# Optimization experiments

Hardware: AMD Instinct MI355X
Metric: run time of the kernel (lower is better)

The kernel has to match this reference:

```python
import jax, jax.numpy as jnp
import numpy as np

B, H, L, DK = 16, 16, 2048, 64   # batch, heads, query len, head dim
LK = 4096                        # original key length
C = 10                           # num_clusters
LKS = 2 * int(np.log(LK))        # shrunk key length = 16


def _lin(x, w, b):
    # torch nn.Linear: y = x @ W^T + b
    return jnp.matmul(x, w.T) + b


def setup_inputs() -> dict:
    key = jax.random.key(0)
    ks = jax.random.split(key, 20)
    s = 0.05
    inp = {
        "Q": jax.random.normal(ks[0], (B, H, L, DK), jnp.float32),
        "K": jax.random.normal(ks[1], (B, H, LK, DK), jnp.float32),
        "V": jax.random.normal(ks[2], (B, H, LK, DK), jnp.float32),
        # shrink_k / shrink_v: Linear(l_k, 2*log(l_k))
        "shrink_k_w": jax.random.normal(ks[3], (LKS, LK), jnp.float32) * s,
        "shrink_k_b": jax.random.normal(ks[4], (LKS,), jnp.float32) * s,
        "shrink_v_w": jax.random.normal(ks[5], (LKS, LK), jnp.float32) * s,
        "shrink_v_b": jax.random.normal(ks[6], (LKS,), jnp.float32) * s,
        # proj_to_cluster_k: Linear(batch_size, num_clusters) + ReLU
        "proj_w": jax.random.normal(ks[7], (C, B), jnp.float32) * s,
        "proj_b": jax.random.normal(ks[8], (C,), jnp.float32) * s,
        "ck_w": jax.random.normal(ks[9], (C, C), jnp.float32) * s,
        "ck_b": jax.random.normal(ks[10], (C,), jnp.float32) * s,
        "cq_w": jax.random.normal(ks[11], (C, C), jnp.float32) * s,
        "cq_b": jax.random.normal(ks[12], (C,), jnp.float32) * s,
        "mu_w": jax.random.normal(ks[13], (C, C), jnp.float32) * s,
        "mu_b": jax.random.normal(ks[14], (C,), jnp.float32) * s,
        "sig_w": jax.random.normal(ks[15], (C, C), jnp.float32) * s,
        "sig_b": jax.random.normal(ks[16], (C,), jnp.float32) * s,
    }
    return inp


def reference(Q, K, V, shrink_k_w, shrink_k_b, shrink_v_w, shrink_v_b,
              proj_w, proj_b, ck_w, ck_b, cq_w, cq_b, mu_w, mu_b, sig_w, sig_b):
    b = Q.shape[0]
    # shrink along key sequence dim: (b,h,lk,d) -> (b,h,LKS,d)
    Ks = jnp.einsum('bhkd,sk->bhsd', K, shrink_k_w) + shrink_k_b[:, None]
    Vs = jnp.einsum('bhkd,sk->bhsd', V, shrink_v_w) + shrink_v_b[:, None]

    # pad + unfold over the batch dim: window j of K_padded[w:w+b]
    K_padded = jnp.concatenate([jnp.zeros_like(Ks), Ks[1:]], axis=0)  # (2b-1,h,LKS,d)
    idx = jnp.arange(b)[:, None] + jnp.arange(b)[None, :]             # (b, b)
    K_unfold = jnp.moveaxis(K_padded[idx], 1, -1)                     # (b,h,LKS,d,b)

    cluster_k_p = jax.nn.relu(_lin(K_unfold, proj_w, proj_b))         # (b,h,LKS,d,C)
    cluster_k = jax.nn.softmax(_lin(cluster_k_p, ck_w, ck_b), axis=-1)
    cluster_q = jax.nn.softmax(_lin(cluster_k_p, cq_w, cq_b), axis=-1)

    mu = _lin(cluster_q, mu_w, mu_b)
    sigma = jax.nn.softplus(_lin(cluster_q, sig_w, sig_b))
    # Normal log_prob
    log_prob = (-0.5 * jnp.square((cluster_k - mu) / sigma)
                - jnp.log(sigma) - 0.5 * jnp.log(2.0 * jnp.pi).astype(cluster_k.dtype))
    # torch CrossEntropyLoss with probability targets: class dim = dim 1 (= h)
    logp = jax.nn.log_softmax(cluster_q, axis=1)
    ce = -jnp.mean(jnp.sum(cluster_q * logp, axis=1))
    loss = -jnp.mean(log_prob) + ce

    # per-cluster masked mean over the last dim, vectorized over clusters.
    # where(argmax==i, cluster_q, 0).mean(-1) == onehot(argmax)[...,i] * mean(cluster_q,-1)
    masks = jax.nn.one_hot(jnp.argmax(cluster_q, axis=-1), C, dtype=cluster_q.dtype)  # (b,h,LKS,d,C)
    q_mean = jnp.mean(cluster_q, axis=-1)                                              # (b,h,LKS,d)
    q_sub = masks * q_mean[..., None]                                                  # (b,h,LKS,d,C)

    scores = jnp.einsum('bhqd,bhkdc->cbhqk', Q, q_sub)  # (C,b,h,l,LKS)
    final_score = jnp.max(scores, axis=0)               # (b,h,l,LKS)
    attn = jax.nn.softmax(final_score, axis=-1)
    context = jnp.einsum('bhqk,bhkd->bhqd', attn, Vs)   # (b,h,l,d)
    return context, loss
```

## Files before the change

kernel.cpp:

```cpp
#include <hip/hip_runtime.h>

#define KS_OFF 0
#define VS_OFF 262144
#define QM_OFF 524288
#define AM_OFF 786432
#define LP_OFF 1048576
#define CE_OFF 1048832

typedef __attribute__((ext_vector_type(8))) short short8;
typedef __attribute__((ext_vector_type(4))) float f32x4;

__device__ inline unsigned short bfb(float x) {
  unsigned u = __float_as_uint(x);
  return (unsigned short)((u + 0x7fffu + ((u >> 16) & 1u)) >> 16);
}
__device__ inline unsigned pk2(float a, float b) {
  return (unsigned)bfb(a) | ((unsigned)bfb(b) << 16);
}
__device__ inline float bft(unsigned short h) {
  return __uint_as_float((unsigned)h << 16);
}
__device__ inline void split3(float x, unsigned short& h, unsigned short& m, unsigned short& l) {
  unsigned u = __float_as_uint(x);
  h = (unsigned short)(u >> 16);
  float r = x - bft(h);
  m = (unsigned short)(__float_as_uint(r) >> 16);
  float r2 = r - bft(m);
  l = bfb(r2);
}
__device__ inline void gload16(const void* g, void* l) {
  __builtin_amdgcn_global_load_lds(
      (const __attribute__((address_space(1))) unsigned*)g,
      (__attribute__((address_space(3))) unsigned*)l, 16, 0, 0);
}

__global__ __launch_bounds__(256) void k_shrink6(
    const float* __restrict__ K, const float* __restrict__ V,
    const float* __restrict__ skw, const float* __restrict__ svw,
    float* __restrict__ part)
{
  int blk = blockIdx.x;
  int q = blk & 3;
  int bh = (blk >> 2) & 255;
  int tensor = blk >> 10;
  const float* __restrict__ src = (tensor ? V : K) + (size_t)bh * (4096 * 64);
  const float* __restrict__ w   = tensor ? svw : skw;
  float* __restrict__ dst = part + (size_t)blk * 1024;

  int t = threadIdx.x;
  int wv = t >> 6;
  int l = t & 63;
  int l15 = l & 15;
  int kg = l >> 4;
  int lr4 = l >> 4;
  union Frag { unsigned u[4]; short8 s8; };

  __shared__ float shm[16384];

#define STAGE(buf, sub) do {                                                  \
    const float* gs = src + (size_t)(q * 1024 + (sub) * 128) * 64;            \
    _Pragma("unroll")                                                         \
    for (int i = 0; i < 8; ++i) {                                             \
      int ch = wv * 8 + i;                                                    \
      int row = ch * 4 + lr4;                                                 \
      int s16 = (l & 15) ^ (((row >> 3) & 3) << 2);                           \
      gload16(gs + (size_t)row * 64 + s16 * 4, &shm[(buf) * 8192 + ch * 256]);\
    } } while (0)

  f32x4 acc[4];
#pragma unroll
  for (int nt = 0; nt < 4; ++nt) acc[nt] = (f32x4){0.f, 0.f, 0.f, 0.f};

  const float* __restrict__ wrow = w + l15 * 4096 + kg * 8;

  STAGE(0, 0);
  int kk0 = q * 32 + wv;
  float4 wa_c = *(const float4*)(wrow + kk0 * 32);
  float4 wb_c = *(const float4*)(wrow + kk0 * 32 + 4);
  __syncthreads();

  for (int sub = 0; sub < 8; ++sub) {
    int cur = sub & 1;
    if (sub < 7) STAGE(cur ^ 1, sub + 1);
    float4 wa_n, wb_n;
    if (sub < 7) {
      int kkn = q * 32 + (sub + 1) * 4 + wv;
      wa_n = *(const float4*)(wrow + kkn * 32);
      wb_n = *(const float4*)(wrow + kkn * 32 + 4);
    }

    float we[8] = {wa_c.x, wa_c.y, wa_c.z, wa_c.w, wb_c.x, wb_c.y, wb_c.z, wb_c.w};
    Frag ah, am, al;
#pragma unroll
    for (int e = 0; e < 4; ++e) {
      unsigned short h0, m0, l0, h1, m1, l1;
      split3(we[2 * e], h0, m0, l0);
      split3(we[2 * e + 1], h1, m1, l1);
      ah.u[e] = (unsigned)h0 | ((unsigned)h1 << 16);
      am.u[e] = (unsigned)m0 | ((unsigned)m1 << 16);
      al.u[e] = (unsigned)l0 | ((unsigned)l1 << 16);
    }

    const float* __restrict__ stage = &shm[cur * 8192];
#pragma unroll
    for (int nt = 0; nt < 4; ++nt) {
      float v[8];
#pragma unroll
      for (int j = 0; j < 8; ++j) {
        int row = wv * 32 + kg * 8 + j;
        int col = (nt * 16 + l15) ^ (((row >> 3) & 3) << 4);
        v[j] = stage[row * 64 + col];
      }
      Frag bh, bm, bl;
#pragma unroll
      for (int e = 0; e < 4; ++e) {
        unsigned short h0, m0, l0, h1, m1, l1;
        split3(v[2 * e], h0, m0, l0);
        split3(v[2 * e + 1], h1, m1, l1);
        bh.u[e] = (unsigned)h0 | ((unsigned)h1 << 16);
        bm.u[e] = (unsigned)m0 | ((unsigned)m1 << 16);
        bl.u[e] = (unsigned)l0 | ((unsigned)l1 << 16);
      }
      acc[nt] = __builtin_amdgcn_mfma_f32_16x16x32_bf16(ah.s8, bh.s8, acc[nt], 0, 0, 0);
      acc[nt] = __builtin_amdgcn_mfma_f32_16x16x32_bf16(ah.s8, bm.s8, acc[nt], 0, 0, 0);
      acc[nt] = __builtin_amdgcn_mfma_f32_16x16x32_bf16(am.s8, bh.s8, acc[nt], 0, 0, 0);
      acc[nt] = __builtin_amdgcn_mfma_f32_16x16x32_bf16(ah.s8, bl.s8, acc[nt], 0, 0, 0);
      acc[nt] = __builtin_amdgcn_mfma_f32_16x16x32_bf16(al.s8, bh.s8, acc[nt], 0, 0, 0);
      acc[nt] = __builtin_amdgcn_mfma_f32_16x16x32_bf16(am.s8, bm.s8, acc[nt], 0, 0, 0);
    }

    if (sub < 7) { wa_c = wa_n; wb_c = wb_n; }
    __syncthreads();
  }

  int g4 = kg * 4;
#pragma unroll
  for (int nt = 0; nt < 4; ++nt)
#pragma unroll
    for (int r = 0; r < 4; ++r)
      shm[wv * 1024 + (g4 + r) * 64 + nt * 16 + l15] = acc[nt][r];
  __syncthreads();
  for (int p = t; p < 1024; p += 256)
    dst[p] = shm[p] + shm[1024 + p] + shm[2048 + p] + shm[3072 + p];
#undef STAGE
}

__global__ __launch_bounds__(256) void k_shrink_red(
    const float* __restrict__ part, const float* __restrict__ skb,
    const float* __restrict__ svb, float* __restrict__ ws)
{
  int blk = blockIdx.x;
  int tensor = blk >> 8;
  int bh = blk & 255;
  const float* __restrict__ p0 = part + ((size_t)(tensor * 1024 + bh * 4)) * 1024;
  const float* __restrict__ bias = tensor ? svb : skb;
  float* __restrict__ dst = ws + (tensor ? VS_OFF : KS_OFF) + bh * 1024;
  for (int p = threadIdx.x; p < 1024; p += 256)
    dst[p] = ((p0[p] + p0[1024 + p]) + (p0[2048 + p] + p0[3072 + p])) + bias[p >> 6];
}

__global__ __launch_bounds__(1024) void k_cluster(
    const float* __restrict__ pw, const float* __restrict__ pb,
    const float* __restrict__ ckw, const float* __restrict__ ckb,
    const float* __restrict__ cqw, const float* __restrict__ cqb,
    const float* __restrict__ muw, const float* __restrict__ mub,
    const float* __restrict__ sgw, const float* __restrict__ sgb,
    float* __restrict__ ws)
{
  int bidx = blockIdx.x >> 4;
  int sIdx = blockIdx.x & 15;
  int t = threadIdx.x;
  int h = t >> 6, d = t & 63;

  __shared__ float wgt[610];
  __shared__ float cqs[16 * 64 * 10];
  if (t < 160) wgt[t] = pw[t];
  else if (t < 170) wgt[t] = pb[t - 160];
  else if (t < 270) wgt[t] = ckw[t - 170];
  else if (t < 280) wgt[t] = ckb[t - 270];
  else if (t < 380) wgt[t] = cqw[t - 280];
  else if (t < 390) wgt[t] = cqb[t - 380];
  else if (t < 490) wgt[t] = muw[t - 390];
  else if (t < 500) wgt[t] = mub[t - 490];
  else if (t < 600) wgt[t] = sgw[t - 500];
  else if (t < 610) wgt[t] = sgb[t - 600];
  __syncthreads();

  const float* __restrict__ Ks = ws + KS_OFF;

  float ckp[10];
#pragma unroll
  for (int c = 0; c < 10; ++c) ckp[c] = wgt[160 + c];
  for (int m = 1; m <= bidx; ++m) {
    float kv = Ks[((m * 16 + h) * 16 + sIdx) * 64 + d];
    int j = m + 15 - bidx;
#pragma unroll
    for (int c = 0; c < 10; ++c) ckp[c] = fmaf(kv, wgt[c * 16 + j], ckp[c]);
  }
#pragma unroll
  for (int c = 0; c < 10; ++c) ckp[c] = fmaxf(ckp[c], 0.f);

  float zk[10], zq[10];
#pragma unroll
  for (int c = 0; c < 10; ++c) { zk[c] = wgt[270 + c]; zq[c] = wgt[380 + c]; }
#pragma unroll
  for (int j = 0; j < 10; ++j) {
    float v = ckp[j];
#pragma unroll
    for (int c = 0; c < 10; ++c) {
      zk[c] = fmaf(v, wgt[170 + c * 10 + j], zk[c]);
      zq[c] = fmaf(v, wgt[280 + c * 10 + j], zq[c]);
    }
  }
  float mk = zk[0], mq = zq[0];
#pragma unroll
  for (int c = 1; c < 10; ++c) { mk = fmaxf(mk, zk[c]); mq = fmaxf(mq, zq[c]); }
  float sk = 0.f, sq = 0.f;
#pragma unroll
  for (int c = 0; c < 10; ++c) {
    zk[c] = expf(zk[c] - mk); sk += zk[c];
    zq[c] = expf(zq[c] - mq); sq += zq[c];
  }
  float rik = 1.f / sk, riq = 1.f / sq;
#pragma unroll
  for (int c = 0; c < 10; ++c) { zk[c] *= rik; zq[c] *= riq; }

  float mu[10], sgz[10];
#pragma unroll
  for (int c = 0; c < 10; ++c) { mu[c] = wgt[490 + c]; sgz[c] = wgt[600 + c]; }
#pragma unroll
  for (int j = 0; j < 10; ++j) {
    float v = zq[j];
#pragma unroll
    for (int c = 0; c < 10; ++c) {
      mu[c]  = fmaf(v, wgt[390 + c * 10 + j], mu[c]);
      sgz[c] = fmaf(v, wgt[500 + c * 10 + j], sgz[c]);
    }
  }
  float lp = 0.f, qmean = 0.f, best = zq[0];
  int amax = 0;
#pragma unroll
  for (int c = 0; c < 10; ++c) {
    float x = sgz[c];
    float sg = (x > 20.f) ? x : log1pf(expf(x));
    float zr = (zk[c] - mu[c]) / sg;
    lp += -0.5f * zr * zr - logf(sg);
    qmean += zq[c];
    if (c > 0 && zq[c] > best) { best = zq[c]; amax = c; }
  }
  lp -= 10.f * 0.91893853320467274f;
  qmean *= 0.1f;

  int pos = ((bidx * 16 + h) * 16 + sIdx) * 64 + d;
  ws[QM_OFF + pos] = qmean;
  ((int*)ws)[AM_OFF + pos] = amax;
#pragma unroll
  for (int c = 0; c < 10; ++c) cqs[(h * 64 + d) * 10 + c] = zq[c];
  __syncthreads();

  float ce = 0.f;
  if (t < 640) {
    int dd = t / 10, cc = t - dd * 10;
    float x[16];
#pragma unroll
    for (int hh = 0; hh < 16; ++hh) x[hh] = cqs[(hh * 64 + dd) * 10 + cc];
    float mx = x[0];
#pragma unroll
    for (int hh = 1; hh < 16; ++hh) mx = fmaxf(mx, x[hh]);
    float sum = 0.f;
#pragma unroll
    for (int hh = 0; hh < 16; ++hh) sum += expf(x[hh] - mx);
    float lse = mx + logf(sum);
#pragma unroll
    for (int hh = 0; hh < 16; ++hh) ce += x[hh] * (x[hh] - lse);
  }

#pragma unroll
  for (int o = 1; o < 64; o <<= 1) { lp += __shfl_xor(lp, o); ce += __shfl_xor(ce, o); }
  __shared__ float redw[16][2];
  if ((t & 63) == 0) { redw[t >> 6][0] = lp; redw[t >> 6][1] = ce; }
  __syncthreads();
  if (t == 0) {
    float Ls = 0.f, Cs = 0.f;
#pragma unroll
    for (int i = 0; i < 16; ++i) { Ls += redw[i][0]; Cs += redw[i][1]; }
    ws[LP_OFF + blockIdx.x] = Ls;
    ws[CE_OFF + blockIdx.x] = Cs;
  }
}

__global__ __launch_bounds__(512, 2) void k_attn(
    const float* __restrict__ Q, float* __restrict__ out,
    const float* __restrict__ ws)
{
  int bid = blockIdx.x;
  int bh = bid >> 3;
  int eighth = bid & 7;
  int t = threadIdx.x;
  int wv = t >> 6;
  int l = t & 63;
  int l15 = l & 15;
  int sbase = (l >> 4) * 8;
  int g4 = (l >> 4) * 4;

  __shared__ unsigned short Gm[10][16][72];
  __shared__ float Vs_l[1024];
  __shared__ unsigned short attn_l[8][16][32];

  const float* __restrict__ qmp = ws + QM_OFF + bh * 1024;
  const int* __restrict__ amp = (const int*)ws + AM_OFF + bh * 1024;
  const float* __restrict__ vsp = ws + VS_OFF + bh * 1024;

  const float* __restrict__ qbp =
      Q + ((size_t)bh * 2048 + eighth * 256 + wv * 32 + l15) * 64 + sbase;
  float4 q4[2][4];
#pragma unroll
  for (int e = 0; e < 4; ++e)
    q4[0][e] = *(const float4*)(qbp + (e >> 1) * 32 + (e & 1) * 4);

  for (int i = t; i < 5760; i += 512) ((unsigned*)Gm)[i] = 0u;
  for (int i = t; i < 2048; i += 512) ((unsigned*)attn_l)[i] = 0u;
  for (int i = t; i < 1024; i += 512) Vs_l[i] = vsp[i];
  __syncthreads();
  for (int p = t; p < 1024; p += 512) {
    int s = p >> 6, dd = p & 63;
    Gm[amp[p]][s][dd] = bfb(qmp[p]);
  }
  __syncthreads();

  union Frag { unsigned u[4]; short8 s8; };

  Frag vf[4];
#pragma unroll
  for (int dt = 0; dt < 4; ++dt) {
#pragma unroll
    for (int e2 = 0; e2 < 4; ++e2) {
      int s0 = sbase + e2 * 2;
      float a = (s0 < 16) ? Vs_l[s0 * 64 + dt * 16 + l15] : 0.f;
      float b = (s0 + 1 < 16) ? Vs_l[(s0 + 1) * 64 + dt * 16 + l15] : 0.f;
      vf[dt].u[e2] = pk2(a, b);
    }
  }

#pragma unroll
  for (int tt = 0; tt < 2; ++tt) {
    int qbase = eighth * 256 + wv * 32 + tt * 16;
    if (tt == 0) {
#pragma unroll
      for (int e = 0; e < 4; ++e)
        q4[1][e] = *(const float4*)(qbp + 1024 + (e >> 1) * 32 + (e & 1) * 4);
    }

    Frag bf[2];
#pragma unroll
    for (int ks = 0; ks < 2; ++ks) {
      float4 a = q4[tt][ks * 2];
      float4 b2 = q4[tt][ks * 2 + 1];
      bf[ks].u[0] = pk2(a.x, a.y);
      bf[ks].u[1] = pk2(a.z, a.w);
      bf[ks].u[2] = pk2(b2.x, b2.y);
      bf[ks].u[3] = pk2(b2.z, b2.w);
    }

    f32x4 acc[10];
#pragma unroll
    for (int c = 0; c < 10; ++c) acc[c] = (f32x4){0.f, 0.f, 0.f, 0.f};
#pragma unroll
    for (int ks = 0; ks < 2; ++ks) {
#pragma unroll
      for (int c = 0; c < 10; ++c) {
        short8 af = *(const short8*)(const void*)&Gm[c][l15][sbase + ks * 32];
        acc[c] = __builtin_amdgcn_mfma_f32_16x16x32_bf16(af, bf[ks].s8, acc[c], 0, 0, 0);
      }
    }
    f32x4 fs = acc[0];
#pragma unroll
    for (int c = 1; c < 10; ++c) {
      fs.x = fmaxf(fs.x, acc[c].x); fs.y = fmaxf(fs.y, acc[c].y);
      fs.z = fmaxf(fs.z, acc[c].z); fs.w = fmaxf(fs.w, acc[c].w);
    }
    float mx = fmaxf(fmaxf(fs.x, fs.y), fmaxf(fs.z, fs.w));
    mx = fmaxf(mx, __shfl_xor(mx, 16));
    mx = fmaxf(mx, __shfl_xor(mx, 32));
    float e0 = __expf(fs.x - mx), e1 = __expf(fs.y - mx),
          e2 = __expf(fs.z - mx), e3 = __expf(fs.w - mx);
    float ssum = e0 + e1 + e2 + e3;
    ssum += __shfl_xor(ssum, 16);
    ssum += __shfl_xor(ssum, 32);
    float inv = 1.f / ssum;
    unsigned* awp = (unsigned*)&attn_l[wv][l15][g4];
    awp[0] = pk2(e0 * inv, e1 * inv);
    awp[1] = pk2(e2 * inv, e3 * inv);
    short8 b2f = *(const short8*)(const void*)&attn_l[wv][l15][sbase];
#pragma unroll
    for (int dt = 0; dt < 4; ++dt) {
      f32x4 ct = (f32x4){0.f, 0.f, 0.f, 0.f};
      ct = __builtin_amdgcn_mfma_f32_16x16x32_bf16(vf[dt].s8, b2f, ct, 0, 0, 0);
      float* op = out + ((size_t)bh * 2048 + qbase + l15) * 64 + dt * 16 + g4;
      *(f32x4*)op = ct;
    }
  }

  if (bid == 0 && t == 0) {
    float Ls = 0.f, Cs = 0.f;
    for (int i = 0; i < 256; ++i) { Ls += ws[LP_OFF + i]; Cs += ws[CE_OFF + i]; }
    out[33554432] = -Ls / 2621440.f - Cs / 163840.f;
  }
}

extern "C" void kernel_launch(void* const* d_in, const int* in_sizes, int n_in,
                              void* d_out, int out_size, void* d_ws, size_t ws_size,
                              hipStream_t stream) {
  const float* Q   = (const float*)d_in[0];
  const float* K   = (const float*)d_in[1];
  const float* V   = (const float*)d_in[2];
  const float* skw = (const float*)d_in[3];
  const float* skb = (const float*)d_in[4];
  const float* svw = (const float*)d_in[5];
  const float* svb = (const float*)d_in[6];
  const float* pw  = (const float*)d_in[7];
  const float* pb  = (const float*)d_in[8];
  const float* ckw = (const float*)d_in[9];
  const float* ckb = (const float*)d_in[10];
  const float* cqw = (const float*)d_in[11];
  const float* cqb = (const float*)d_in[12];
  const float* muw = (const float*)d_in[13];
  const float* mub = (const float*)d_in[14];
  const float* sgw = (const float*)d_in[15];
  const float* sgb = (const float*)d_in[16];
  float* out = (float*)d_out;
  float* ws  = (float*)d_ws;

  hipLaunchKernelGGL(k_shrink6, dim3(2048), dim3(256), 0, stream, K, V, skw, svw, out);
  hipLaunchKernelGGL(k_shrink_red, dim3(512), dim3(256), 0, stream, out, skb, svb, ws);
  hipLaunchKernelGGL(k_cluster, dim3(256), dim3(1024), 0, stream,
                     pw, pb, ckw, ckb, cqw, cqb, muw, mub, sgw, sgb, ws);
  hipLaunchKernelGGL(k_attn, dim3(2048), dim3(512), 0, stream, Q, out, ws);
}
```

Baseline: 294.4 us.

## Process a whole (b,h) slice per attn block with double-buffered Q prefetch

k_attn now launches one 1024-thread block per batch-head instead of eight 512-thread blocks. Each wave walks 8 query tiles of 16 rows and prefetches the next tile's Q into a ping-pong register buffer. This is meant to build the per-cluster Gm table and the Vs/attn LDS setup once per head rather than eight times, and to overlap Q loads with compute. In exchange only 256 blocks run, one per CU with launch bounds (1024,1), which lowers occupancy and may hurt latency hiding on a device with 256 CUs.

```diff
diff --git a/kernel.cpp b/kernel.cpp
--- a/kernel.cpp
+++ b/kernel.cpp
@@ -289,13 +289,11 @@
   }
 }
 
-__global__ __launch_bounds__(512, 2) void k_attn(
+__global__ __launch_bounds__(1024, 1) void k_attn(
     const float* __restrict__ Q, float* __restrict__ out,
     const float* __restrict__ ws)
 {
-  int bid = blockIdx.x;
-  int bh = bid >> 3;
-  int eighth = bid & 7;
+  int bh = blockIdx.x;
   int t = threadIdx.x;
   int wv = t >> 6;
   int l = t & 63;
@@ -305,27 +303,25 @@
 
   __shared__ unsigned short Gm[10][16][72];
   __shared__ float Vs_l[1024];
-  __shared__ unsigned short attn_l[8][16][32];
+  __shared__ unsigned short attn_l[16][16][32];
 
   const float* __restrict__ qmp = ws + QM_OFF + bh * 1024;
   const int* __restrict__ amp = (const int*)ws + AM_OFF + bh * 1024;
   const float* __restrict__ vsp = ws + VS_OFF + bh * 1024;
 
   const float* __restrict__ qbp =
-      Q + ((size_t)bh * 2048 + eighth * 256 + wv * 32 + l15) * 64 + sbase;
-  float4 q4[2][4];
+      Q + ((size_t)bh * 2048 + wv * 128 + l15) * 64 + sbase;
+
+  float4 qA[4], qB[4];
 #pragma unroll
   for (int e = 0; e < 4; ++e)
-    q4[0][e] = *(const float4*)(qbp + (e >> 1) * 32 + (e & 1) * 4);
-
-  for (int i = t; i < 5760; i += 512) ((unsigned*)Gm)[i] = 0u;
-  for (int i = t; i < 2048; i += 512) ((unsigned*)attn_l)[i] = 0u;
-  for (int i = t; i < 1024; i += 512) Vs_l[i] = vsp[i];
-  __syncthreads();
-  for (int p = t; p < 1024; p += 512) {
-    int s = p >> 6, dd = p & 63;
-    Gm[amp[p]][s][dd] = bfb(qmp[p]);
-  }
+    qA[e] = *(const float4*)(qbp + (e >> 1) * 32 + (e & 1) * 4);
+
+  for (int i = t; i < 5760; i += 1024) ((unsigned*)Gm)[i] = 0u;
+  for (int i = t; i < 4096; i += 1024) ((unsigned*)attn_l)[i] = 0u;
+  Vs_l[t] = vsp[t];
+  __syncthreads();
+  Gm[amp[t]][t >> 6][t & 63] = bfb(qmp[t]);
   __syncthreads();
 
   union Frag { unsigned u[4]; short8 s8; };
@@ -343,19 +339,21 @@
   }
 
 #pragma unroll
-  for (int tt = 0; tt < 2; ++tt) {
-    int qbase = eighth * 256 + wv * 32 + tt * 16;
-    if (tt == 0) {
+  for (int tt = 0; tt < 8; ++tt) {
+    if (tt < 7) {
+      const float* np = qbp + (size_t)(tt + 1) * 1024;
+      float4* nxt = (tt & 1) ? qA : qB;
 #pragma unroll
       for (int e = 0; e < 4; ++e)
-        q4[1][e] = *(const float4*)(qbp + 1024 + (e >> 1) * 32 + (e & 1) * 4);
-    }
+        nxt[e] = *(const float4*)(np + (e >> 1) * 32 + (e & 1) * 4);
+    }
+    const float4* cur = (tt & 1) ? qB : qA;
 
     Frag bf[2];
 #pragma unroll
     for (int ks = 0; ks < 2; ++ks) {
-      float4 a = q4[tt][ks * 2];
-      float4 b2 = q4[tt][ks * 2 + 1];
+      float4 a = cur[ks * 2];
+      float4 b2 = cur[ks * 2 + 1];
       bf[ks].u[0] = pk2(a.x, a.y);
       bf[ks].u[1] = pk2(a.z, a.w);
       bf[ks].u[2] = pk2(b2.x, b2.y);
@@ -396,12 +394,12 @@
     for (int dt = 0; dt < 4; ++dt) {
       f32x4 ct = (f32x4){0.f, 0.f, 0.f, 0.f};
       ct = __builtin_amdgcn_mfma_f32_16x16x32_bf16(vf[dt].s8, b2f, ct, 0, 0, 0);
-      float* op = out + ((size_t)bh * 2048 + qbase + l15) * 64 + dt * 16 + g4;
+      float* op = out + ((size_t)bh * 2048 + wv * 128 + tt * 16 + l15) * 64 + dt * 16 + g4;
       *(f32x4*)op = ct;
     }
   }
 
-  if (bid == 0 && t == 0) {
+  if (bh == 0 && t == 0) {
     float Ls = 0.f, Cs = 0.f;
     for (int i = 0; i < 256; ++i) { Ls += ws[LP_OFF + i]; Cs += ws[CE_OFF + i]; }
     out[33554432] = -Ls / 2621440.f - Cs / 163840.f;
@@ -435,5 +433,5 @@
   hipLaunchKernelGGL(k_shrink_red, dim3(512), dim3(256), 0, stream, out, skb, svb, ws);
   hipLaunchKernelGGL(k_cluster, dim3(256), dim3(1024), 0, stream,
                      pw, pb, ckw, ckb, cqw, cqb, muw, mub, sgw, sgb, ws);
-  hipLaunchKernelGGL(k_attn, dim3(2048), dim3(512), 0, stream, Q, out, ws);
-}
+  hipLaunchKernelGGL(k_attn, dim3(256), dim3(1024), 0, stream, Q, out, ws);
+}
```

After: 303.3 us. +3.0%, slower.

## Replace shared LDS double-buffer with per-wave register-staged loads and nontemporal accesses

Applied to the files above, without the earlier changes.

The shrink kernel stops using async global-to-LDS loads into a block-wide double buffer with a __syncthreads per step. Each wave now prefetches its own 32-row slice into registers with nontemporal loads, writes it to a private LDS region, and reads it back without block barriers. This halves the LDS footprint, which can raise occupancy, at the cost of more registers and an extra register-to-LDS write. The attention kernel also switches its Q loads and output stores to nontemporal to reduce cache pollution from streamed data.

```diff
diff --git a/kernel.cpp b/kernel.cpp
--- a/kernel.cpp
+++ b/kernel.cpp
@@ -28,13 +28,8 @@
   float r2 = r - bft(m);
   l = bfb(r2);
 }
-__device__ inline void gload16(const void* g, void* l) {
-  __builtin_amdgcn_global_load_lds(
-      (const __attribute__((address_space(1))) unsigned*)g,
-      (__attribute__((address_space(3))) unsigned*)l, 16, 0, 0);
-}
-
-__global__ __launch_bounds__(256) void k_shrink6(
+
+__global__ __launch_bounds__(256) void k_shrink7(
     const float* __restrict__ K, const float* __restrict__ V,
     const float* __restrict__ skw, const float* __restrict__ svw,
     float* __restrict__ part)
@@ -55,33 +50,36 @@
   int lr4 = l >> 4;
   union Frag { unsigned u[4]; short8 s8; };
 
-  __shared__ float shm[16384];
-
-#define STAGE(buf, sub) do {                                                  \
-    const float* gs = src + (size_t)(q * 1024 + (sub) * 128) * 64;            \
+  __shared__ float shm[8192];
+  float* __restrict__ my = shm + wv * 2048;
+
+#define STAGE_LOAD(sub) do {                                                  \
+    const float* gs = src + (size_t)(q * 1024 + (sub) * 128 + wv * 32) * 64;  \
     _Pragma("unroll")                                                         \
     for (int i = 0; i < 8; ++i) {                                             \
-      int ch = wv * 8 + i;                                                    \
-      int row = ch * 4 + lr4;                                                 \
-      int s16 = (l & 15) ^ (((row >> 3) & 3) << 2);                           \
-      gload16(gs + (size_t)row * 64 + s16 * 4, &shm[(buf) * 8192 + ch * 256]);\
+      int rl = i * 4 + lr4;                                                   \
+      int s16 = (l & 15) ^ (((rl >> 3) & 3) << 2);                            \
+      ld[i] = __builtin_nontemporal_load((const f32x4*)(gs + rl * 64 + s16 * 4)); \
     } } while (0)
 
+  f32x4 ld[8];
   f32x4 acc[4];
 #pragma unroll
   for (int nt = 0; nt < 4; ++nt) acc[nt] = (f32x4){0.f, 0.f, 0.f, 0.f};
 
   const float* __restrict__ wrow = w + l15 * 4096 + kg * 8;
 
-  STAGE(0, 0);
+  STAGE_LOAD(0);
   int kk0 = q * 32 + wv;
   float4 wa_c = *(const float4*)(wrow + kk0 * 32);
   float4 wb_c = *(const float4*)(wrow + kk0 * 32 + 4);
-  __syncthreads();
 
   for (int sub = 0; sub < 8; ++sub) {
-    int cur = sub & 1;
-    if (sub < 7) STAGE(cur ^ 1, sub + 1);
+#pragma unroll
+    for (int i = 0; i < 8; ++i)
+      *(f32x4*)&my[(i * 4 + lr4) * 64 + (l & 15) * 4] = ld[i];
+
+    if (sub < 7) STAGE_LOAD(sub + 1);
     float4 wa_n, wb_n;
     if (sub < 7) {
       int kkn = q * 32 + (sub + 1) * 4 + wv;
@@ -101,15 +99,14 @@
       al.u[e] = (unsigned)l0 | ((unsigned)l1 << 16);
     }
 
-    const float* __restrict__ stage = &shm[cur * 8192];
 #pragma unroll
     for (int nt = 0; nt < 4; ++nt) {
       float v[8];
 #pragma unroll
       for (int j = 0; j < 8; ++j) {
-        int row = wv * 32 + kg * 8 + j;
-        int col = (nt * 16 + l15) ^ (((row >> 3) & 3) << 4);
-        v[j] = stage[row * 64 + col];
+        int rl = kg * 8 + j;
+        int col = (nt * 16 + l15) ^ (((rl >> 3) & 3) << 4);
+        v[j] = my[rl * 64 + col];
       }
       Frag bh, bm, bl;
 #pragma unroll
@@ -130,9 +127,9 @@
     }
 
     if (sub < 7) { wa_c = wa_n; wb_c = wb_n; }
-    __syncthreads();
-  }
-
+  }
+
+  __syncthreads();
   int g4 = kg * 4;
 #pragma unroll
   for (int nt = 0; nt < 4; ++nt)
@@ -142,7 +139,7 @@
   __syncthreads();
   for (int p = t; p < 1024; p += 256)
     dst[p] = shm[p] + shm[1024 + p] + shm[2048 + p] + shm[3072 + p];
-#undef STAGE
+#undef STAGE_LOAD
 }
 
 __global__ __launch_bounds__(256) void k_shrink_red(
@@ -313,10 +310,11 @@
 
   const float* __restrict__ qbp =
       Q + ((size_t)bh * 2048 + eighth * 256 + wv * 32 + l15) * 64 + sbase;
-  float4 q4[2][4];
+  f32x4 q4[2][4];
 #pragma unroll
   for (int e = 0; e < 4; ++e)
-    q4[0][e] = *(const float4*)(qbp + (e >> 1) * 32 + (e & 1) * 4);
+    q4[0][e] = __builtin_nontemporal_load(
+        (const f32x4*)(qbp + (e >> 1) * 32 + (e & 1) * 4));
 
   for (int i = t; i < 5760; i += 512) ((unsigned*)Gm)[i] = 0u;
   for (int i = t; i < 2048; i += 512) ((unsigned*)attn_l)[i] = 0u;
@@ -348,14 +346,15 @@
     if (tt == 0) {
 #pragma unroll
       for (int e = 0; e < 4; ++e)
-        q4[1][e] = *(const float4*)(qbp + 1024 + (e >> 1) * 32 + (e & 1) * 4);
+        q4[1][e] = __builtin_nontemporal_load(
+            (const f32x4*)(qbp + 1024 + (e >> 1) * 32 + (e & 1) * 4));
     }
 
     Frag bf[2];
 #pragma unroll
     for (int ks = 0; ks < 2; ++ks) {
-      float4 a = q4[tt][ks * 2];
-      float4 b2 = q4[tt][ks * 2 + 1];
+      f32x4 a = q4[tt][ks * 2];
+      f32x4 b2 = q4[tt][ks * 2 + 1];
       bf[ks].u[0] = pk2(a.x, a.y);
       bf[ks].u[1] = pk2(a.z, a.w);
       bf[ks].u[2] = pk2(b2.x, b2.y);
@@ -397,7 +396,7 @@
       f32x4 ct = (f32x4){0.f, 0.f, 0.f, 0.f};
       ct = __builtin_amdgcn_mfma_f32_16x16x32_bf16(vf[dt].s8, b2f, ct, 0, 0, 0);
       float* op = out + ((size_t)bh * 2048 + qbase + l15) * 64 + dt * 16 + g4;
-      *(f32x4*)op = ct;
+      __builtin_nontemporal_store(ct, (f32x4*)op);
     }
   }
 
@@ -431,7 +430,7 @@
   float* out = (float*)d_out;
   float* ws  = (float*)d_ws;
 
-  hipLaunchKernelGGL(k_shrink6, dim3(2048), dim3(256), 0, stream, K, V, skw, svw, out);
+  hipLaunchKernelGGL(k_shrink7, dim3(2048), dim3(256), 0, stream, K, V, skw, svw, out);
   hipLaunchKernelGGL(k_shrink_red, dim3(512), dim3(256), 0, stream, out, skb, svb, ws);
   hipLaunchKernelGGL(k_cluster, dim3(256), dim3(1024), 0, stream,
                      pw, pb, ckw, ckb, cqw, cqb, muw, mub, sgw, sgb, ws);
```

After: 276.8 us. 1.06x faster.
